# Performance work log

Hardware: AMD Instinct MI355X
Metric: run time of the kernel (lower is better)

## Reference

```python
import math
import jax, jax.numpy as jnp
import numpy as np

N = 2048
HID = 1024
ALPHA = 0.5
BETA = 0.1  # greedy term is zero when coords is None


def setup_inputs() -> dict:
    key = jax.random.key(0)
    k1, k2, k3, k4 = jax.random.split(key, 4)
    node_emb = jax.random.normal(k1, (N, HID), jnp.float32)
    demands = jax.random.uniform(k2, (N,), jnp.float32)  # each < 1 << capacity
    # query_net: Linear(hid+2 -> hid); key_net: Linear(hid -> hid)
    Wq = jax.random.normal(k3, (HID, HID + 2), jnp.float32) / math.sqrt(HID + 2)
    bq = jnp.zeros((HID,), jnp.float32)
    Wk = jax.random.normal(k4, (HID, HID), jnp.float32) / math.sqrt(HID)
    bk = jnp.zeros((HID,), jnp.float32)
    return {"node_emb": node_emb, "demands": demands, "Wq": Wq, "bq": bq,
            "Wk": Wk, "bk": bk, "capacity": 40, "depot_idx": 0}


def _decode(node_emb, demands, Wq, bq, Wk, bk, capacity, depot_idx):
    n, h = node_emb.shape
    cap = jnp.float32(capacity)
    inv_sqrt = 1.0 / math.sqrt(h)
    # key_net is a per-node linear map: precompute once (same math as per-step gather+linear)
    K = node_emb @ Wk.T + bk  # [N, H]
    idx = jnp.arange(n)
    # demands < 1, capacity = 40 => >= 39 customers per route => few depot returns;
    # T = N + N//8 safely bounds customer picks + route-closing depot emissions.
    T = n + n // 8
    visited0 = jnp.zeros((n,), bool).at[depot_idx].set(True)

    def step(carry, _):
        visited, load, last, done = carry
        feasible = (~visited) & (demands <= load)
        has_cand = jnp.any(feasible)
        # context = [emb(last), load/capacity, avgd]; avgd = 0 since coords is None
        ctx = jnp.concatenate([node_emb[last],
                               jnp.stack([load / cap, jnp.float32(0.0)])])
        q = Wq @ ctx + bq                      # [H]
        s = ALPHA * ((K @ q) * inv_sqrt)       # [N] scores over all nodes
        s_m = jnp.where(feasible, s, -jnp.inf)
        cand = jnp.argmax(s_m)
        take = has_cand & (~done)
        nxt = jnp.where(take, cand, depot_idx).astype(jnp.int32)
        step_score = jnp.where(take, s[cand], jnp.float32(0.0))
        visited = visited | ((idx == cand) & take)
        load = jnp.where(take, load - demands[cand], cap)  # route end resets load
        done = done | ((~take) & jnp.all(visited))
        return (visited, load, nxt, done), (nxt, step_score)

    carry0 = (visited0, cap, jnp.int32(depot_idx), jnp.bool_(False))
    _, (seq, scores) = jax.lax.scan(step, carry0, None, length=T)
    tour = jnp.concatenate([jnp.array([depot_idx], seq.dtype), seq])  # [T+1]
    return tour, scores


def reference(node_emb, demands, Wq, bq, Wk, bk, capacity, depot_idx):
    # tour: flat visitation order; routes are the segments between depot occurrences
    # (trailing depots are padding once all customers are served).
    # scores: selected decoder score at each step (0 at depot/padding steps).
    return _decode(node_emb, demands, Wq, bq, Wk, bk, capacity, depot_idx)
```

## Files before the change

kernel.cpp:

```cpp
#include <hip/hip_runtime.h>
#include <hip/hip_bf16.h>


#define NN 2048
#define HH 1024
#define TSTEPS (NN + NN / 8)
#define TILE 64
#define KT 16
#define KCAND 128

__global__ __launch_bounds__(256) void prep_wqh(const float* __restrict__ Wq,
                                                float* __restrict__ Wqh) {
  int id = blockIdx.x * 256 + threadIdx.x;
  int r = id >> 10, c = id & 1023;
  Wqh[id] = Wq[r * (HH + 2) + c];
}

__global__ __launch_bounds__(256) void gemm_nt(const float* __restrict__ A, int lda,
                                               const float* __restrict__ B, int ldb,
                                               float* __restrict__ C, int ldc,
                                               int K, const float* __restrict__ bias) {
  __shared__ float As[KT][TILE + 4];
  __shared__ float Bs[KT][TILE + 4];
  const int i0 = blockIdx.y * TILE;
  const int j0 = blockIdx.x * TILE;
  const int t = threadIdx.x;
  const int srow = t >> 2, sq = t & 3;
  const int tx = t & 15, ty = t >> 4;
  float acc[4][4] = {};
  for (int k0 = 0; k0 < K; k0 += KT) {
    float4 av = *(const float4*)&A[(size_t)(i0 + srow) * lda + k0 + sq * 4];
    float4 bv = *(const float4*)&B[(size_t)(j0 + srow) * ldb + k0 + sq * 4];
    __syncthreads();
    As[sq * 4 + 0][srow] = av.x; As[sq * 4 + 1][srow] = av.y;
    As[sq * 4 + 2][srow] = av.z; As[sq * 4 + 3][srow] = av.w;
    Bs[sq * 4 + 0][srow] = bv.x; Bs[sq * 4 + 1][srow] = bv.y;
    Bs[sq * 4 + 2][srow] = bv.z; Bs[sq * 4 + 3][srow] = bv.w;
    __syncthreads();
#pragma unroll
    for (int k = 0; k < KT; ++k) {
      float4 a4 = *(const float4*)&As[k][ty * 4];
      float4 b4 = *(const float4*)&Bs[k][tx * 4];
      float a[4] = {a4.x, a4.y, a4.z, a4.w};
      float b[4] = {b4.x, b4.y, b4.z, b4.w};
#pragma unroll
      for (int m = 0; m < 4; ++m)
#pragma unroll
        for (int n = 0; n < 4; ++n) acc[m][n] = fmaf(a[m], b[n], acc[m][n]);
    }
  }
  float bb[4] = {0.f, 0.f, 0.f, 0.f};
  if (bias) {
#pragma unroll
    for (int n = 0; n < 4; ++n) bb[n] = bias[j0 + tx * 4 + n];
  }
#pragma unroll
  for (int m = 0; m < 4; ++m) {
    float4 st = {acc[m][0] + bb[0], acc[m][1] + bb[1], acc[m][2] + bb[2], acc[m][3] + bb[3]};
    *(float4*)&C[(size_t)(i0 + ty * 4 + m) * ldc + j0 + tx * 4] = st;
  }
}

__global__ __launch_bounds__(64) void uv_k(const float* __restrict__ Kmat,
                                           const float* __restrict__ Wq,
                                           const float* __restrict__ bq,
                                           float* __restrict__ u, float* __restrict__ v) {
  int i = blockIdx.x;
  int lane = threadIdx.x;
  float su = 0.f, sv = 0.f;
#pragma unroll
  for (int m = 0; m < HH / 64; ++m) {
    int j = lane + 64 * m;
    float kv = Kmat[(size_t)i * HH + j];
    su = fmaf(kv, Wq[(size_t)j * (HH + 2) + HH], su);
    sv = fmaf(kv, bq[j], sv);
  }
#pragma unroll
  for (int off = 32; off; off >>= 1) {
    su += __shfl_down(su, off, 64);
    sv += __shfl_down(sv, off, 64);
  }
  if (lane == 0) { u[i] = su; v[i] = sv; }
}

__global__ __launch_bounds__(256) void umax_k(const float* __restrict__ u,
                                              float* __restrict__ umaxp) {
  __shared__ float sm[256];
  int t = threadIdx.x;
  float m = 0.f;
  for (int i = t; i < NN; i += 256) m = fmaxf(m, fabsf(u[i]));
  sm[t] = m;
  __syncthreads();
  for (int s = 128; s; s >>= 1) {
    if (t < s) sm[t] = fmaxf(sm[t], sm[t + s]);
    __syncthreads();
  }
  if (t == 0) *umaxp = sm[0];
}

__device__ __forceinline__ unsigned f2key(float f) {
  unsigned x = __float_as_uint(f);
  return x ^ ((x >> 31) ? 0xFFFFFFFFu : 0x80000000u);
}
__device__ __forceinline__ float key2f(unsigned k) {
  unsigned x = (k & 0x80000000u) ? (k ^ 0x80000000u) : ~k;
  return __uint_as_float(x);
}
__global__ __launch_bounds__(256) void prep_cand(const float* __restrict__ GT,
                                                 uint2* __restrict__ cand,
                                                 float* __restrict__ thr) {
  __shared__ float rowv[NN];
  __shared__ int hist[256];
  __shared__ int s_d, s_need, s_gt, s_eq;
  const int row = blockIdx.x, t = threadIdx.x;
  for (int i = t; i < NN; i += 256) rowv[i] = GT[(size_t)row * NN + i];
  __syncthreads();
  unsigned prefix = 0;
  int need = KCAND;
  for (int pass = 0; pass < 4; ++pass) {
    hist[t] = 0;
    __syncthreads();
    const int shift = 24 - 8 * pass;
    for (int i = t; i < NN; i += 256) {
      unsigned k = f2key(rowv[i]);
      if (pass == 0 || (k >> (shift + 8)) == (prefix >> (shift + 8)))
        atomicAdd(&hist[(k >> shift) & 0xFF], 1);
    }
    __syncthreads();
    if (t == 0) {
      int cum = 0, d = 255;
      for (; d > 0; --d) {
        if (cum + hist[d] >= need) break;
        cum += hist[d];
      }
      s_d = d;
      s_need = need - cum;
    }
    __syncthreads();
    prefix |= ((unsigned)s_d) << shift;
    need = s_need;
    __syncthreads();
  }
  const unsigned thrk = prefix;
  if (t == 0) { s_gt = 0; s_eq = 0; thr[row] = key2f(thrk); }
  __syncthreads();
  for (int i = t; i < NN; i += 256) {
    if (f2key(rowv[i]) > thrk) {
      int p = atomicAdd(&s_gt, 1);
      cand[(size_t)row * KCAND + p] = make_uint2(__float_as_uint(rowv[i]), (unsigned)i);
    }
  }
  __syncthreads();
  const int cgt = s_gt;
  for (int i = t; i < NN; i += 256) {
    if (f2key(rowv[i]) == thrk) {
      int p = atomicAdd(&s_eq, 1);
      if (p < KCAND - cgt)
        cand[(size_t)row * KCAND + cgt + p] = make_uint2(__float_as_uint(rowv[i]), (unsigned)i);
    }
  }
}

__global__ __launch_bounds__(256) void warm_k(const float* __restrict__ a, int n,
                                              const float* __restrict__ b, int m,
                                              float* __restrict__ sink) {
  float s = 0.f;
  const float4* a4 = (const float4*)a;
  for (int i = threadIdx.x; i < n / 4; i += 256) {
    float4 x = a4[i];
    s += x.x + x.y + x.z + x.w;
  }
  for (int i = threadIdx.x; i < m; i += 256) s += b[i];
  if (s == 1.2345e-30f) sink[blockIdx.x] = s;
}

#define DPP_MERGE2(CTRL)                                                      \
  {                                                                           \
    int ovb = __builtin_amdgcn_update_dpp(                                    \
        (int)0xFF800000, __float_as_int(bv), (CTRL), 0xf, 0xf, false);        \
    int oib = __builtin_amdgcn_update_dpp(                                    \
        0x7fffffff, bi, (CTRL), 0xf, 0xf, false);                             \
    float ov = __int_as_float(ovb);                                           \
    if (ov > bv || (ov == bv && oib < bi)) { bv = ov; bi = oib; }             \
  }

__global__ __launch_bounds__(64, 1) void decode(const float* __restrict__ GT,
                                                const uint2* __restrict__ cand,
                                                const float* __restrict__ thrp,
                                                const float* __restrict__ umaxp,
                                                const float* __restrict__ u,
                                                const float* __restrict__ demands,
                                                const int* __restrict__ capp,
                                                const int* __restrict__ depotp,
                                                float* __restrict__ out) {
  __shared__ __align__(16) float s_dem[NN];
  __shared__ __align__(16) float s_dd[NN];
  __shared__ __align__(16) float s_u[NN];
  __shared__ __align__(16) uint4 s_dcand[KCAND / 2];
  __shared__ __align__(16) float s_tour[TSTEPS + 1];
  __shared__ __align__(16) float s_lr[TSTEPS];

  const int lane = threadIdx.x;
  const int depot = *depotp;
  const float capf = (float)(*capp);
  const float umaxv = *umaxp;
  const float INF = __builtin_inff();
  const float NEGINF = -INF;
  const float C0 = 0.015625f;
  const float MARGIN = 0.5f;

  for (int i = lane; i < NN; i += 64) {
    float d = demands[i];
    s_dem[i] = d;
    s_dd[i] = d;
    s_u[i] = u[i];
  }
  const uint4* dc4 = (const uint4*)(cand + (size_t)depot * KCAND);
  for (int i = lane; i < KCAND / 2; i += 64) s_dcand[i] = dc4[i];
  const float thrd = thrp[depot];
  __syncthreads();
  if (lane == 0) {
    s_dd[depot] = INF;
    s_tour[0] = (float)depot;
  }

  float uu[32];
#pragma unroll
  for (int r = 0; r < 8; ++r) {
    float4 u4 = ((const float4*)u)[r * 64 + lane];
    uu[r * 4 + 0] = u4.x; uu[r * 4 + 1] = u4.y;
    uu[r * 4 + 2] = u4.z; uu[r * 4 + 3] = u4.w;
  }

  const float4* dd4 = (const float4*)s_dd;

  int done = 0, ntaken = 0, lasts = depot;
  float load = capf;
  float lr = load / capf;
  float thrcur = thrd;
  uint4 ca = dc4[lane];

  for (int step = 0; step < TSTEPS; ++step) {
    if (done) {
      const float df = (float)depot;
      for (int q = step + lane; q < TSTEPS; q += 64) {
        s_tour[1 + q] = df;
        s_lr[q] = -1.0f;
      }
      break;
    }
    float bv = NEGINF;
    int bi = 0x7fffffff;
    {
      float g0 = __uint_as_float(ca.x); int i0 = (int)ca.y;
      float g1 = __uint_as_float(ca.z); int i1 = (int)ca.w;
      float d0 = s_dd[i0], u0 = s_u[i0];
      float d1 = s_dd[i1], u1 = s_u[i1];
      float t0 = fmaf(u0, lr, g0);
      float t1 = fmaf(u1, lr, g1);
      if ((d0 <= load) && (t0 > bv || (t0 == bv && i0 < bi))) { bv = t0; bi = i0; }
      if ((d1 <= load) && (t1 > bv || (t1 == bv && i1 < bi))) { bv = t1; bi = i1; }
    }
    DPP_MERGE2(0x111); DPP_MERGE2(0x112); DPP_MERGE2(0x114);
    DPP_MERGE2(0x118); DPP_MERGE2(0x142); DPP_MERGE2(0x143);
    float rbv = __int_as_float(__builtin_amdgcn_readlane(__float_as_int(bv), 63));
    int rbi = __builtin_amdgcn_readlane(bi, 63);

    const float B = fmaf(lr, umaxv, thrcur) + MARGIN;
    int take, nxt;
    if (rbv > B) {
      take = 1; nxt = rbi;
    } else {
      const float4* rowp = (const float4*)(GT + (size_t)lasts * NN);
      float bv = NEGINF;
      int bi = NN;
#pragma unroll
      for (int r = 0; r < 8; ++r) {
        float4 g4 = rowp[r * 64 + lane];
        float4 d4 = dd4[r * 64 + lane];
        float gl[4] = {g4.x, g4.y, g4.z, g4.w};
        float dl[4] = {d4.x, d4.y, d4.z, d4.w};
        float cv = NEGINF;
        int cj = 0;
#pragma unroll
        for (int j = 0; j < 4; ++j) {
          float tt = fmaf(uu[r * 4 + j], lr, gl[j]);
          bool feas = (dl[j] <= load);
          if (feas && tt > cv) { cv = tt; cj = j; }
        }
        if (cv > bv) { bv = cv; bi = 4 * (r * 64 + lane) + cj; }
      }
      DPP_MERGE2(0x111); DPP_MERGE2(0x112); DPP_MERGE2(0x114);
      DPP_MERGE2(0x118); DPP_MERGE2(0x142); DPP_MERGE2(0x143);
      float fbv = __int_as_float(__builtin_amdgcn_readlane(__float_as_int(bv), 63));
      rbi = __builtin_amdgcn_readlane(bi, 63);
      take = (fbv > NEGINF);
      nxt = take ? rbi : depot;
    }

    if (nxt == depot) {
      ca = s_dcand[lane];
      thrcur = thrd;
    } else {
      const uint4* rc4 = (const uint4*)(cand + (size_t)nxt * KCAND);
      ca = rc4[lane];
      thrcur = thrp[nxt];
    }

    if (lane == 0) {
      s_tour[1 + step] = (float)nxt;
      s_lr[step] = take ? lr : -1.0f;
    }
    if (take) {
      load = load - s_dem[rbi];
      ntaken++;
      if (lane == 0) s_dd[rbi] = INF;
    } else {
      load = capf;
      if (ntaken == NN - 1) done = 1;
    }
    lasts = nxt;
    lr = load / capf;
  }

  for (int i = lane; i <= TSTEPS; i += 64) out[i] = s_tour[i];
  for (int s = lane; s < TSTEPS; s += 64) {
    float lrs = s_lr[s];
    float sc = 0.0f;
    if (lrs >= 0.0f) {
      int lastI = (int)s_tour[s];
      int biI = (int)s_tour[s + 1];
      float g = GT[(size_t)lastI * NN + biI];
      sc = fmaf(u[biI], lrs, g) * C0;
    }
    out[1 + TSTEPS + s] = sc;
  }
}

extern "C" void kernel_launch(void* const* d_in, const int* in_sizes, int n_in,
                              void* d_out, int out_size, void* d_ws, size_t ws_size,
                              hipStream_t stream) {
  const float* emb     = (const float*)d_in[0];
  const float* demands = (const float*)d_in[1];
  const float* Wq      = (const float*)d_in[2];
  const float* bq      = (const float*)d_in[3];
  const float* Wk      = (const float*)d_in[4];
  const float* bk      = (const float*)d_in[5];
  const int* cap       = (const int*)d_in[6];
  const int* depot     = (const int*)d_in[7];
  float* out           = (float*)d_out;

  char* ws = (char*)d_ws;
  float* Kmat = (float*)(ws);
  float* Z    = (float*)(ws + ((size_t)8 << 20));
  float* GT   = (float*)(ws + ((size_t)16 << 20));
  float* Wqh  = (float*)(ws + ((size_t)32 << 20));
  float* u    = (float*)(ws + ((size_t)36 << 20));
  float* v    = (float*)(ws + ((size_t)36 << 20) + 8192);
  float* thr  = (float*)(ws + ((size_t)36 << 20) + 16384);
  float* umax = (float*)(ws + ((size_t)36 << 20) + 24576);
  float* sink = (float*)(ws + ((size_t)36 << 20) + 32768);
  uint2* cnd  = (uint2*)Wqh;

  hipLaunchKernelGGL(prep_wqh, dim3(4096), dim3(256), 0, stream, Wq, Wqh);
  hipLaunchKernelGGL(gemm_nt, dim3(HH / TILE, NN / TILE), dim3(256), 0, stream,
                     emb, HH, Wk, HH, Kmat, HH, HH, bk);
  hipLaunchKernelGGL(gemm_nt, dim3(HH / TILE, NN / TILE), dim3(256), 0, stream,
                     emb, HH, Wqh, HH, Z, HH, HH, (const float*)nullptr);
  hipLaunchKernelGGL(uv_k, dim3(NN), dim3(64), 0, stream, Kmat, Wq, bq, u, v);
  hipLaunchKernelGGL(umax_k, dim3(1), dim3(256), 0, stream, u, umax);
  hipLaunchKernelGGL(gemm_nt, dim3(NN / TILE, NN / TILE), dim3(256), 0, stream,
                     Z, HH, Kmat, HH, GT, NN, HH, v);
  hipLaunchKernelGGL(prep_cand, dim3(NN), dim3(256), 0, stream, GT, cnd, thr);
  hipLaunchKernelGGL(warm_k, dim3(128), dim3(256), 0, stream,
                     (const float*)cnd, NN * KCAND * 2, thr, NN, sink);
  hipLaunchKernelGGL(decode, dim3(1), dim3(64), 0, stream, GT, cnd, thr, umax,
                     u, demands, cap, depot, out);
}
```

Measured before the change: 2.046 ms.

## Add bf16 top-5 per-row candidate tier in LDS before top-128 and full-row fallback

A new kernel builds each row's top-5 candidates, packed as bf16 score plus index, and decode keeps the whole table in LDS. Each step first tries a top-2 DPP merge over these five entries and accepts the winner only when it clears the runner-up and the 5th threshold by an error margin. Otherwise it falls back to the top-128 candidate list, now software-prefetched a step ahead, and then to the full row scan. This aims to cut the per-step global-memory latency on the serial decode path. The error margin and tie handling add correctness risk, and tour and score outputs now go through global buffers.

Measured after the change: 2.163 ms. +5.7%, slower.

```diff
diff --git a/kernel.cpp b/kernel.cpp
--- a/kernel.cpp
+++ b/kernel.cpp
@@ -7,7 +7,8 @@
 #define TSTEPS (NN + NN / 8)
 #define TILE 64
 #define KT 16
-#define KCAND 128
+#define KMID 128
+#define TSTR 6
 
 __global__ __launch_bounds__(256) void prep_wqh(const float* __restrict__ Wq,
                                                 float* __restrict__ Wqh) {
@@ -83,8 +84,16 @@
   if (lane == 0) { u[i] = su; v[i] = sv; }
 }
 
+__device__ __forceinline__ unsigned short f2bf_rn(float f) {
+  unsigned x = __float_as_uint(f);
+  unsigned r = ((x >> 16) & 1u) + 0x7fffu;
+  return (unsigned short)((x + r) >> 16);
+}
+
 __global__ __launch_bounds__(256) void umax_k(const float* __restrict__ u,
-                                              float* __restrict__ umaxp) {
+                                              float* __restrict__ umaxp,
+                                              unsigned* __restrict__ gmaxA,
+                                              unsigned* __restrict__ ub16) {
   __shared__ float sm[256];
   int t = threadIdx.x;
   float m = 0.f;
@@ -95,7 +104,9 @@
     if (t < s) sm[t] = fmaxf(sm[t], sm[t + s]);
     __syncthreads();
   }
-  if (t == 0) *umaxp = sm[0];
+  if (t == 0) { *umaxp = sm[0]; *gmaxA = 0u; }
+  for (int i = t; i < NN / 2; i += 256)
+    ub16[i] = (unsigned)f2bf_rn(u[2 * i]) | ((unsigned)f2bf_rn(u[2 * i + 1]) << 16);
 }
 
 __device__ __forceinline__ unsigned f2key(float f) {
@@ -116,7 +127,7 @@
   for (int i = t; i < NN; i += 256) rowv[i] = GT[(size_t)row * NN + i];
   __syncthreads();
   unsigned prefix = 0;
-  int need = KCAND;
+  int need = KMID;
   for (int pass = 0; pass < 4; ++pass) {
     hist[t] = 0;
     __syncthreads();
@@ -147,7 +158,7 @@
   for (int i = t; i < NN; i += 256) {
     if (f2key(rowv[i]) > thrk) {
       int p = atomicAdd(&s_gt, 1);
-      cand[(size_t)row * KCAND + p] = make_uint2(__float_as_uint(rowv[i]), (unsigned)i);
+      cand[(size_t)row * KMID + p] = make_uint2(__float_as_uint(rowv[i]), (unsigned)i);
     }
   }
   __syncthreads();
@@ -155,10 +166,46 @@
   for (int i = t; i < NN; i += 256) {
     if (f2key(rowv[i]) == thrk) {
       int p = atomicAdd(&s_eq, 1);
-      if (p < KCAND - cgt)
-        cand[(size_t)row * KCAND + cgt + p] = make_uint2(__float_as_uint(rowv[i]), (unsigned)i);
-    }
-  }
+      if (p < KMID - cgt)
+        cand[(size_t)row * KMID + cgt + p] = make_uint2(__float_as_uint(rowv[i]), (unsigned)i);
+    }
+  }
+}
+
+#define DPP_MERGE2(CTRL)                                                      \
+  {                                                                           \
+    int ovb = __builtin_amdgcn_update_dpp(                                    \
+        (int)0xFF800000, __float_as_int(bv), (CTRL), 0xf, 0xf, false);        \
+    int oib = __builtin_amdgcn_update_dpp(                                    \
+        0x7fffffff, bi, (CTRL), 0xf, 0xf, false);                             \
+    float ov = __int_as_float(ovb);                                           \
+    if (ov > bv || (ov == bv && oib < bi)) { bv = ov; bi = oib; }             \
+  }
+
+__global__ __launch_bounds__(64) void prep_top5(const uint2* __restrict__ cand,
+                                                unsigned* __restrict__ c5,
+                                                unsigned* __restrict__ gmaxA) {
+  const int row = blockIdx.x, lane = threadIdx.x;
+  uint2 e0 = cand[(size_t)row * KMID + lane];
+  uint2 e1 = cand[(size_t)row * KMID + 64 + lane];
+  float g0 = __uint_as_float(e0.x), g1 = __uint_as_float(e1.x);
+  float am = 0.f;
+  for (int k = 0; k < 5; ++k) {
+    float bv; int bi;
+    if (g0 >= g1) { bv = g0; bi = lane * 2; } else { bv = g1; bi = lane * 2 + 1; }
+    DPP_MERGE2(0x111); DPP_MERGE2(0x112); DPP_MERGE2(0x114);
+    DPP_MERGE2(0x118); DPP_MERGE2(0x142); DPP_MERGE2(0x143);
+    float wv = __int_as_float(__builtin_amdgcn_readlane(__float_as_int(bv), 63));
+    int wenc = __builtin_amdgcn_readlane(bi, 63);
+    if (lane == (wenc >> 1)) {
+      unsigned idx = (wenc & 1) ? e1.y : e0.y;
+      c5[row * TSTR + k] = ((unsigned)f2bf_rn(wv) << 16) | (idx & 0xffffu);
+      if (k == 4) c5[row * TSTR + 5] = __float_as_uint(wv);
+      if (wenc & 1) g1 = -__builtin_inff(); else g0 = -__builtin_inff();
+    }
+    am = fmaxf(am, fabsf(wv));
+  }
+  if (lane == 0) atomicMax(gmaxA, __float_as_uint(am));
 }
 
 __global__ __launch_bounds__(256) void warm_k(const float* __restrict__ a, int n,
@@ -174,55 +221,55 @@
   if (s == 1.2345e-30f) sink[blockIdx.x] = s;
 }
 
-#define DPP_MERGE2(CTRL)                                                      \
+#define TOP2_MERGE(CTRL)                                                      \
   {                                                                           \
-    int ovb = __builtin_amdgcn_update_dpp(                                    \
-        (int)0xFF800000, __float_as_int(bv), (CTRL), 0xf, 0xf, false);        \
-    int oib = __builtin_amdgcn_update_dpp(                                    \
-        0x7fffffff, bi, (CTRL), 0xf, 0xf, false);                             \
-    float ov = __int_as_float(ovb);                                           \
-    if (ov > bv || (ov == bv && oib < bi)) { bv = ov; bi = oib; }             \
+    int ov1b = __builtin_amdgcn_update_dpp(                                   \
+        (int)0xFF800000, __float_as_int(v1), (CTRL), 0xf, 0xf, false);        \
+    int oi1b = __builtin_amdgcn_update_dpp(                                   \
+        0x7fffffff, i1, (CTRL), 0xf, 0xf, false);                             \
+    int ov2b = __builtin_amdgcn_update_dpp(                                   \
+        (int)0xFF800000, __float_as_int(v2), (CTRL), 0xf, 0xf, false);        \
+    float ov1 = __int_as_float(ov1b), ov2 = __int_as_float(ov2b);             \
+    float vmax = fmaxf(v1, ov1), vmin = fminf(v1, ov1);                       \
+    v2 = fmaxf(vmin, fmaxf(v2, ov2));                                         \
+    i1 = (ov1 > v1) ? oi1b : ((ov1 < v1) ? i1 : min(i1, oi1b));               \
+    v1 = vmax;                                                                \
   }
 
 __global__ __launch_bounds__(64, 1) void decode(const float* __restrict__ GT,
                                                 const uint2* __restrict__ cand,
                                                 const float* __restrict__ thrp,
+                                                const unsigned* __restrict__ c5g,
+                                                const unsigned* __restrict__ ub16,
+                                                const unsigned* __restrict__ gmaxA,
                                                 const float* __restrict__ umaxp,
                                                 const float* __restrict__ u,
                                                 const float* __restrict__ demands,
                                                 const int* __restrict__ capp,
                                                 const int* __restrict__ depotp,
+                                                int* __restrict__ tourW,
+                                                float* __restrict__ lrW,
                                                 float* __restrict__ out) {
-  __shared__ __align__(16) float s_dem[NN];
+  __shared__ __align__(16) unsigned s_c5[NN * TSTR];
   __shared__ __align__(16) float s_dd[NN];
-  __shared__ __align__(16) float s_u[NN];
-  __shared__ __align__(16) uint4 s_dcand[KCAND / 2];
-  __shared__ __align__(16) float s_tour[TSTEPS + 1];
-  __shared__ __align__(16) float s_lr[TSTEPS];
+  __shared__ __align__(16) unsigned short s_ub[NN];
 
   const int lane = threadIdx.x;
   const int depot = *depotp;
   const float capf = (float)(*capp);
   const float umaxv = *umaxp;
+  const float gmaxv = __uint_as_float(*gmaxA);
   const float INF = __builtin_inff();
   const float NEGINF = -INF;
   const float C0 = 0.015625f;
-  const float MARGIN = 0.5f;
-
-  for (int i = lane; i < NN; i += 64) {
-    float d = demands[i];
-    s_dem[i] = d;
-    s_dd[i] = d;
-    s_u[i] = u[i];
-  }
-  const uint4* dc4 = (const uint4*)(cand + (size_t)depot * KCAND);
-  for (int i = lane; i < KCAND / 2; i += 64) s_dcand[i] = dc4[i];
-  const float thrd = thrp[depot];
+  const float EPST = (gmaxv + umaxv) * 0.0021f + 0.02f;
+
+  for (int i = lane; i < NN * TSTR / 4; i += 64)
+    ((uint4*)s_c5)[i] = ((const uint4*)c5g)[i];
+  for (int i = lane; i < NN; i += 64) s_dd[i] = demands[i];
+  for (int i = lane; i < NN / 2; i += 64) ((unsigned*)s_ub)[i] = ub16[i];
   __syncthreads();
-  if (lane == 0) {
-    s_dd[depot] = INF;
-    s_tour[0] = (float)depot;
-  }
+  if (lane == 0) s_dd[depot] = INF;
 
   float uu[32];
 #pragma unroll
@@ -231,107 +278,125 @@
     uu[r * 4 + 0] = u4.x; uu[r * 4 + 1] = u4.y;
     uu[r * 4 + 2] = u4.z; uu[r * 4 + 3] = u4.w;
   }
-
   const float4* dd4 = (const float4*)s_dd;
 
   int done = 0, ntaken = 0, lasts = depot;
   float load = capf;
   float lr = load / capf;
-  float thrcur = thrd;
-  uint4 ca = dc4[lane];
+
+  uint4 pf0 = *(const uint4*)(cand + (size_t)depot * KMID + lane * 2);
+  uint4 pf1 = pf0;
+  float thr0 = thrp[depot], thr1 = thr0;
 
   for (int step = 0; step < TSTEPS; ++step) {
     if (done) {
-      const float df = (float)depot;
       for (int q = step + lane; q < TSTEPS; q += 64) {
-        s_tour[1 + q] = df;
-        s_lr[q] = -1.0f;
+        tourW[q] = depot;
+        lrW[q] = -1.0f;
       }
       break;
     }
-    float bv = NEGINF;
-    int bi = 0x7fffffff;
-    {
-      float g0 = __uint_as_float(ca.x); int i0 = (int)ca.y;
-      float g1 = __uint_as_float(ca.z); int i1 = (int)ca.w;
-      float d0 = s_dd[i0], u0 = s_u[i0];
-      float d1 = s_dd[i1], u1 = s_u[i1];
-      float t0 = fmaf(u0, lr, g0);
-      float t1 = fmaf(u1, lr, g1);
-      if ((d0 <= load) && (t0 > bv || (t0 == bv && i0 < bi))) { bv = t0; bi = i0; }
-      if ((d1 <= load) && (t1 > bv || (t1 == bv && i1 < bi))) { bv = t1; bi = i1; }
-    }
-    DPP_MERGE2(0x111); DPP_MERGE2(0x112); DPP_MERGE2(0x114);
-    DPP_MERGE2(0x118); DPP_MERGE2(0x142); DPP_MERGE2(0x143);
-    float rbv = __int_as_float(__builtin_amdgcn_readlane(__float_as_int(bv), 63));
-    int rbi = __builtin_amdgcn_readlane(bi, 63);
-
-    const float B = fmaf(lr, umaxv, thrcur) + MARGIN;
+    unsigned w = 0;
+    if (lane < 6) w = s_c5[lasts * TSTR + lane];
+    float v1 = NEGINF, v2 = NEGINF;
+    int i1 = 0x7fffffff;
+    if (lane < 5) {
+      int idx = (int)(w & 0xffffu);
+      float gh = __uint_as_float(w & 0xffff0000u);
+      float uh = __uint_as_float(((unsigned)s_ub[idx]) << 16);
+      float d = s_dd[idx];
+      float t = fmaf(uh, lr, gh);
+      if (d <= load) { v1 = t; i1 = idx; }
+    }
+    TOP2_MERGE(0x111); TOP2_MERGE(0x112); TOP2_MERGE(0x114);
+    const float s1 = __int_as_float(__builtin_amdgcn_readlane(__float_as_int(v1), 7));
+    const float s2 = __int_as_float(__builtin_amdgcn_readlane(__float_as_int(v2), 7));
+    const int si = __builtin_amdgcn_readlane(i1, 7);
+    const float thr5v = __uint_as_float(__builtin_amdgcn_readlane((int)w, 5));
+    const float slack = fmaf(lr, umaxv, 0.5f) + EPST;
+
     int take, nxt;
-    if (rbv > B) {
-      take = 1; nxt = rbi;
+    if (s1 - EPST > s2 + EPST && s1 - EPST > thr5v + slack) {
+      take = 1; nxt = si;
     } else {
-      const float4* rowp = (const float4*)(GT + (size_t)lasts * NN);
+      const uint4 c4 = (step & 1) ? pf1 : pf0;
+      const float thrm = (step & 1) ? thr1 : thr0;
       float bv = NEGINF;
-      int bi = NN;
-#pragma unroll
-      for (int r = 0; r < 8; ++r) {
-        float4 g4 = rowp[r * 64 + lane];
-        float4 d4 = dd4[r * 64 + lane];
-        float gl[4] = {g4.x, g4.y, g4.z, g4.w};
-        float dl[4] = {d4.x, d4.y, d4.z, d4.w};
-        float cv = NEGINF;
-        int cj = 0;
-#pragma unroll
-        for (int j = 0; j < 4; ++j) {
-          float tt = fmaf(uu[r * 4 + j], lr, gl[j]);
-          bool feas = (dl[j] <= load);
-          if (feas && tt > cv) { cv = tt; cj = j; }
-        }
-        if (cv > bv) { bv = cv; bi = 4 * (r * 64 + lane) + cj; }
+      int bi = 0x7fffffff;
+      {
+        float g0 = __uint_as_float(c4.x); int j0 = (int)c4.y;
+        float g1 = __uint_as_float(c4.z); int j1 = (int)c4.w;
+        float d0 = s_dd[j0], d1 = s_dd[j1];
+        float ue0 = u[j0], ue1 = u[j1];
+        float t0 = fmaf(ue0, lr, g0);
+        float t1 = fmaf(ue1, lr, g1);
+        if ((d0 <= load) && (t0 > bv || (t0 == bv && j0 < bi))) { bv = t0; bi = j0; }
+        if ((d1 <= load) && (t1 > bv || (t1 == bv && j1 < bi))) { bv = t1; bi = j1; }
       }
       DPP_MERGE2(0x111); DPP_MERGE2(0x112); DPP_MERGE2(0x114);
       DPP_MERGE2(0x118); DPP_MERGE2(0x142); DPP_MERGE2(0x143);
-      float fbv = __int_as_float(__builtin_amdgcn_readlane(__float_as_int(bv), 63));
-      rbi = __builtin_amdgcn_readlane(bi, 63);
-      take = (fbv > NEGINF);
-      nxt = take ? rbi : depot;
-    }
-
-    if (nxt == depot) {
-      ca = s_dcand[lane];
-      thrcur = thrd;
-    } else {
-      const uint4* rc4 = (const uint4*)(cand + (size_t)nxt * KCAND);
-      ca = rc4[lane];
-      thrcur = thrp[nxt];
-    }
-
-    if (lane == 0) {
-      s_tour[1 + step] = (float)nxt;
-      s_lr[step] = take ? lr : -1.0f;
-    }
+      float rbv = __int_as_float(__builtin_amdgcn_readlane(__float_as_int(bv), 63));
+      int rbi = __builtin_amdgcn_readlane(bi, 63);
+      if (rbv > fmaf(lr, umaxv, thrm) + 0.5f) {
+        take = 1; nxt = rbi;
+      } else {
+        const float4* rowp = (const float4*)(GT + (size_t)lasts * NN);
+        float bv = NEGINF;
+        int bi = NN;
+#pragma unroll
+        for (int r = 0; r < 8; ++r) {
+          float4 g4 = rowp[r * 64 + lane];
+          float4 d4 = dd4[r * 64 + lane];
+          float gl[4] = {g4.x, g4.y, g4.z, g4.w};
+          float dl[4] = {d4.x, d4.y, d4.z, d4.w};
+          float cv = NEGINF;
+          int cj = 0;
+#pragma unroll
+          for (int j = 0; j < 4; ++j) {
+            float tt = fmaf(uu[r * 4 + j], lr, gl[j]);
+            bool feas = (dl[j] <= load);
+            if (feas && tt > cv) { cv = tt; cj = j; }
+          }
+          if (cv > bv) { bv = cv; bi = 4 * (r * 64 + lane) + cj; }
+        }
+        DPP_MERGE2(0x111); DPP_MERGE2(0x112); DPP_MERGE2(0x114);
+        DPP_MERGE2(0x118); DPP_MERGE2(0x142); DPP_MERGE2(0x143);
+        float fbv = __int_as_float(__builtin_amdgcn_readlane(__float_as_int(bv), 63));
+        int fbi = __builtin_amdgcn_readlane(bi, 63);
+        take = (fbv > NEGINF);
+        nxt = take ? fbi : depot;
+      }
+    }
+
+    if (lane == 0) { tourW[step] = nxt; lrW[step] = take ? lr : -1.0f; }
     if (take) {
-      load = load - s_dem[rbi];
+      float dsel = s_dd[nxt];
+      load = load - dsel;
       ntaken++;
-      if (lane == 0) s_dd[rbi] = INF;
+      if (lane == 0) s_dd[nxt] = INF;
     } else {
       load = capf;
       if (ntaken == NN - 1) done = 1;
     }
     lasts = nxt;
     lr = load / capf;
-  }
-
-  for (int i = lane; i <= TSTEPS; i += 64) out[i] = s_tour[i];
+
+    uint4 npf = *(const uint4*)(cand + (size_t)lasts * KMID + lane * 2);
+    float nthr = thrp[lasts];
+    if (step & 1) { pf0 = npf; thr0 = nthr; } else { pf1 = npf; thr1 = nthr; }
+  }
+
+  __threadfence();
+  if (lane == 0) out[0] = (float)depot;
   for (int s = lane; s < TSTEPS; s += 64) {
-    float lrs = s_lr[s];
+    int nx = tourW[s];
+    out[1 + s] = (float)nx;
+    float lrs = lrW[s];
     float sc = 0.0f;
     if (lrs >= 0.0f) {
-      int lastI = (int)s_tour[s];
-      int biI = (int)s_tour[s + 1];
-      float g = GT[(size_t)lastI * NN + biI];
-      sc = fmaf(u[biI], lrs, g) * C0;
+      int lastI = (s == 0) ? depot : tourW[s - 1];
+      float g = GT[(size_t)lastI * NN + nx];
+      sc = fmaf(u[nx], lrs, g) * C0;
     }
     out[1 + TSTEPS + s] = sc;
   }
@@ -355,12 +420,18 @@
   float* Z    = (float*)(ws + ((size_t)8 << 20));
   float* GT   = (float*)(ws + ((size_t)16 << 20));
   float* Wqh  = (float*)(ws + ((size_t)32 << 20));
-  float* u    = (float*)(ws + ((size_t)36 << 20));
-  float* v    = (float*)(ws + ((size_t)36 << 20) + 8192);
-  float* thr  = (float*)(ws + ((size_t)36 << 20) + 16384);
-  float* umax = (float*)(ws + ((size_t)36 << 20) + 24576);
-  float* sink = (float*)(ws + ((size_t)36 << 20) + 32768);
-  uint2* cnd  = (uint2*)Wqh;
+  char* ex    = ws + ((size_t)36 << 20);
+  float* u      = (float*)(ex);
+  float* v      = (float*)(ex + 8192);
+  float* thr    = (float*)(ex + 16384);
+  float* umax   = (float*)(ex + 24576);
+  unsigned* gmaxA = (unsigned*)(ex + 24704);
+  float* sink   = (float*)(ex + 24832);
+  unsigned* ub16 = (unsigned*)(ex + 32768);
+  unsigned* c5g  = (unsigned*)(ex + 40960);
+  int* tourW    = (int*)(ex + 40960 + 49152);
+  float* lrW    = (float*)(ex + 40960 + 49152 + 9216);
+  uint2* cnd    = (uint2*)Wqh;
 
   hipLaunchKernelGGL(prep_wqh, dim3(4096), dim3(256), 0, stream, Wq, Wqh);
   hipLaunchKernelGGL(gemm_nt, dim3(HH / TILE, NN / TILE), dim3(256), 0, stream,
@@ -368,12 +439,13 @@
   hipLaunchKernelGGL(gemm_nt, dim3(HH / TILE, NN / TILE), dim3(256), 0, stream,
                      emb, HH, Wqh, HH, Z, HH, HH, (const float*)nullptr);
   hipLaunchKernelGGL(uv_k, dim3(NN), dim3(64), 0, stream, Kmat, Wq, bq, u, v);
-  hipLaunchKernelGGL(umax_k, dim3(1), dim3(256), 0, stream, u, umax);
+  hipLaunchKernelGGL(umax_k, dim3(1), dim3(256), 0, stream, u, umax, gmaxA, ub16);
   hipLaunchKernelGGL(gemm_nt, dim3(NN / TILE, NN / TILE), dim3(256), 0, stream,
                      Z, HH, Kmat, HH, GT, NN, HH, v);
   hipLaunchKernelGGL(prep_cand, dim3(NN), dim3(256), 0, stream, GT, cnd, thr);
+  hipLaunchKernelGGL(prep_top5, dim3(NN), dim3(64), 0, stream, cnd, c5g, gmaxA);
   hipLaunchKernelGGL(warm_k, dim3(128), dim3(256), 0, stream,
-                     (const float*)cnd, NN * KCAND * 2, thr, NN, sink);
-  hipLaunchKernelGGL(decode, dim3(1), dim3(64), 0, stream, GT, cnd, thr, umax,
-                     u, demands, cap, depot, out);
-}
+                     (const float*)cnd, NN * KMID * 2, thr, NN, sink);
+  hipLaunchKernelGGL(decode, dim3(1), dim3(64), 0, stream, GT, cnd, thr, c5g,
+                     ub16, gmaxA, umax, u, demands, cap, depot, tourW, lrW, out);
+}
```

## Pack u and demand into candidate records and prefetch via async LDS loads

Applied to the files above, without the earlier changes.

Candidate entries grow to 16 bytes holding score, index, u and demand, so the decode loop no longer does dependent LDS lookups of u and demand per candidate. The next row's candidates are pulled with global_load_lds into a double buffer in shared memory. Visited state moves to a bitmask, thresholds are read from shared memory, and the tour and lr arrays move from LDS to global scratch. This doubles candidate memory and the warm-up footprint, and the serial decode still waits on vmcnt(0) every step.

After: 2.469 ms. +20.7%, slower.

```diff
diff --git a/kernel.cpp b/kernel.cpp
--- a/kernel.cpp
+++ b/kernel.cpp
@@ -7,7 +7,7 @@
 #define TSTEPS (NN + NN / 8)
 #define TILE 64
 #define KT 16
-#define KCAND 128
+#define KMID 128
 
 __global__ __launch_bounds__(256) void prep_wqh(const float* __restrict__ Wq,
                                                 float* __restrict__ Wqh) {
@@ -107,7 +107,9 @@
   return __uint_as_float(x);
 }
 __global__ __launch_bounds__(256) void prep_cand(const float* __restrict__ GT,
-                                                 uint2* __restrict__ cand,
+                                                 const float* __restrict__ u,
+                                                 const float* __restrict__ dem,
+                                                 uint4* __restrict__ cand,
                                                  float* __restrict__ thr) {
   __shared__ float rowv[NN];
   __shared__ int hist[256];
@@ -116,7 +118,7 @@
   for (int i = t; i < NN; i += 256) rowv[i] = GT[(size_t)row * NN + i];
   __syncthreads();
   unsigned prefix = 0;
-  int need = KCAND;
+  int need = KMID;
   for (int pass = 0; pass < 4; ++pass) {
     hist[t] = 0;
     __syncthreads();
@@ -147,7 +149,9 @@
   for (int i = t; i < NN; i += 256) {
     if (f2key(rowv[i]) > thrk) {
       int p = atomicAdd(&s_gt, 1);
-      cand[(size_t)row * KCAND + p] = make_uint2(__float_as_uint(rowv[i]), (unsigned)i);
+      cand[(size_t)row * KMID + p] =
+          make_uint4(__float_as_uint(rowv[i]), (unsigned)i,
+                     __float_as_uint(u[i]), __float_as_uint(dem[i]));
     }
   }
   __syncthreads();
@@ -155,8 +159,10 @@
   for (int i = t; i < NN; i += 256) {
     if (f2key(rowv[i]) == thrk) {
       int p = atomicAdd(&s_eq, 1);
-      if (p < KCAND - cgt)
-        cand[(size_t)row * KCAND + cgt + p] = make_uint2(__float_as_uint(rowv[i]), (unsigned)i);
+      if (p < KMID - cgt)
+        cand[(size_t)row * KMID + cgt + p] =
+            make_uint4(__float_as_uint(rowv[i]), (unsigned)i,
+                       __float_as_uint(u[i]), __float_as_uint(dem[i]));
     }
   }
 }
@@ -184,21 +190,27 @@
     if (ov > bv || (ov == bv && oib < bi)) { bv = ov; bi = oib; }             \
   }
 
+__device__ __forceinline__ void gload_lds16(const uint4* g, uint4* l) {
+  __builtin_amdgcn_global_load_lds(
+      (const __attribute__((address_space(1))) void*)g,
+      (__attribute__((address_space(3))) void*)l, 16, 0, 0);
+}
+
 __global__ __launch_bounds__(64, 1) void decode(const float* __restrict__ GT,
-                                                const uint2* __restrict__ cand,
+                                                const uint4* __restrict__ cand,
                                                 const float* __restrict__ thrp,
                                                 const float* __restrict__ umaxp,
                                                 const float* __restrict__ u,
                                                 const float* __restrict__ demands,
                                                 const int* __restrict__ capp,
                                                 const int* __restrict__ depotp,
+                                                int* __restrict__ tourW,
+                                                float* __restrict__ lrW,
                                                 float* __restrict__ out) {
-  __shared__ __align__(16) float s_dem[NN];
   __shared__ __align__(16) float s_dd[NN];
-  __shared__ __align__(16) float s_u[NN];
-  __shared__ __align__(16) uint4 s_dcand[KCAND / 2];
-  __shared__ __align__(16) float s_tour[TSTEPS + 1];
-  __shared__ __align__(16) float s_lr[TSTEPS];
+  __shared__ __align__(16) float s_thr[NN];
+  __shared__ __align__(16) unsigned s_vis[NN / 32];
+  __shared__ __align__(16) uint4 s_pf[2][KMID];
 
   const int lane = threadIdx.x;
   const int depot = *depotp;
@@ -207,21 +219,18 @@
   const float INF = __builtin_inff();
   const float NEGINF = -INF;
   const float C0 = 0.015625f;
-  const float MARGIN = 0.5f;
 
   for (int i = lane; i < NN; i += 64) {
-    float d = demands[i];
-    s_dem[i] = d;
-    s_dd[i] = d;
-    s_u[i] = u[i];
-  }
-  const uint4* dc4 = (const uint4*)(cand + (size_t)depot * KCAND);
-  for (int i = lane; i < KCAND / 2; i += 64) s_dcand[i] = dc4[i];
-  const float thrd = thrp[depot];
+    s_dd[i] = demands[i];
+    s_thr[i] = thrp[i];
+  }
+  if (lane == 0) {
+    for (int i = 0; i < NN / 32; ++i) s_vis[i] = 0xFFFFFFFFu;
+  }
   __syncthreads();
   if (lane == 0) {
     s_dd[depot] = INF;
-    s_tour[0] = (float)depot;
+    s_vis[depot >> 5] &= ~(1u << (depot & 31));
   }
 
   float uu[32];
@@ -231,44 +240,49 @@
     uu[r * 4 + 0] = u4.x; uu[r * 4 + 1] = u4.y;
     uu[r * 4 + 2] = u4.z; uu[r * 4 + 3] = u4.w;
   }
-
   const float4* dd4 = (const float4*)s_dd;
 
   int done = 0, ntaken = 0, lasts = depot;
   float load = capf;
   float lr = load / capf;
-  float thrcur = thrd;
-  uint4 ca = dc4[lane];
+
+  gload_lds16(cand + (size_t)depot * KMID + lane, &s_pf[0][0]);
+  gload_lds16(cand + (size_t)depot * KMID + 64 + lane, &s_pf[0][64]);
 
   for (int step = 0; step < TSTEPS; ++step) {
     if (done) {
-      const float df = (float)depot;
       for (int q = step + lane; q < TSTEPS; q += 64) {
-        s_tour[1 + q] = df;
-        s_lr[q] = -1.0f;
+        tourW[q] = depot;
+        lrW[q] = -1.0f;
       }
       break;
     }
+    const int par = step & 1;
+    asm volatile("s_waitcnt vmcnt(0)" ::: "memory");
+    uint4 e0 = s_pf[par][lane];
+    uint4 e1 = s_pf[par][64 + lane];
+
     float bv = NEGINF;
     int bi = 0x7fffffff;
     {
-      float g0 = __uint_as_float(ca.x); int i0 = (int)ca.y;
-      float g1 = __uint_as_float(ca.z); int i1 = (int)ca.w;
-      float d0 = s_dd[i0], u0 = s_u[i0];
-      float d1 = s_dd[i1], u1 = s_u[i1];
+      float g0 = __uint_as_float(e0.x); int j0 = (int)e0.y;
+      float u0 = __uint_as_float(e0.z); float d0 = __uint_as_float(e0.w);
+      float g1 = __uint_as_float(e1.x); int j1 = (int)e1.y;
+      float u1 = __uint_as_float(e1.z); float d1 = __uint_as_float(e1.w);
+      bool f0 = (d0 <= load) && ((s_vis[j0 >> 5] >> (j0 & 31)) & 1u);
+      bool f1 = (d1 <= load) && ((s_vis[j1 >> 5] >> (j1 & 31)) & 1u);
       float t0 = fmaf(u0, lr, g0);
       float t1 = fmaf(u1, lr, g1);
-      if ((d0 <= load) && (t0 > bv || (t0 == bv && i0 < bi))) { bv = t0; bi = i0; }
-      if ((d1 <= load) && (t1 > bv || (t1 == bv && i1 < bi))) { bv = t1; bi = i1; }
+      if (f0 && (t0 > bv || (t0 == bv && j0 < bi))) { bv = t0; bi = j0; }
+      if (f1 && (t1 > bv || (t1 == bv && j1 < bi))) { bv = t1; bi = j1; }
     }
     DPP_MERGE2(0x111); DPP_MERGE2(0x112); DPP_MERGE2(0x114);
     DPP_MERGE2(0x118); DPP_MERGE2(0x142); DPP_MERGE2(0x143);
     float rbv = __int_as_float(__builtin_amdgcn_readlane(__float_as_int(bv), 63));
     int rbi = __builtin_amdgcn_readlane(bi, 63);
 
-    const float B = fmaf(lr, umaxv, thrcur) + MARGIN;
     int take, nxt;
-    if (rbv > B) {
+    if (rbv > fmaf(lr, umaxv, s_thr[lasts]) + 0.5f) {
       take = 1; nxt = rbi;
     } else {
       const float4* rowp = (const float4*)(GT + (size_t)lasts * NN);
@@ -293,28 +307,26 @@
       DPP_MERGE2(0x111); DPP_MERGE2(0x112); DPP_MERGE2(0x114);
       DPP_MERGE2(0x118); DPP_MERGE2(0x142); DPP_MERGE2(0x143);
       float fbv = __int_as_float(__builtin_amdgcn_readlane(__float_as_int(bv), 63));
-      rbi = __builtin_amdgcn_readlane(bi, 63);
+      int fbi = __builtin_amdgcn_readlane(bi, 63);
       take = (fbv > NEGINF);
-      nxt = take ? rbi : depot;
-    }
-
-    if (nxt == depot) {
-      ca = s_dcand[lane];
-      thrcur = thrd;
-    } else {
-      const uint4* rc4 = (const uint4*)(cand + (size_t)nxt * KCAND);
-      ca = rc4[lane];
-      thrcur = thrp[nxt];
-    }
-
-    if (lane == 0) {
-      s_tour[1 + step] = (float)nxt;
-      s_lr[step] = take ? lr : -1.0f;
-    }
+      nxt = take ? fbi : depot;
+    }
+
+    {
+      const uint4* gsrc = cand + (size_t)nxt * KMID + lane;
+      gload_lds16(gsrc, &s_pf[par ^ 1][0]);
+      gload_lds16(gsrc + 64, &s_pf[par ^ 1][64]);
+    }
+
+    if (lane == 0) { tourW[step] = nxt; lrW[step] = take ? lr : -1.0f; }
     if (take) {
-      load = load - s_dem[rbi];
+      float dsel = s_dd[nxt];
+      load = load - dsel;
       ntaken++;
-      if (lane == 0) s_dd[rbi] = INF;
+      if (lane == 0) {
+        s_dd[nxt] = INF;
+        s_vis[nxt >> 5] &= ~(1u << (nxt & 31));
+      }
     } else {
       load = capf;
       if (ntaken == NN - 1) done = 1;
@@ -323,15 +335,17 @@
     lr = load / capf;
   }
 
-  for (int i = lane; i <= TSTEPS; i += 64) out[i] = s_tour[i];
+  __threadfence();
+  if (lane == 0) out[0] = (float)depot;
   for (int s = lane; s < TSTEPS; s += 64) {
-    float lrs = s_lr[s];
+    int nx = tourW[s];
+    out[1 + s] = (float)nx;
+    float lrs = lrW[s];
     float sc = 0.0f;
     if (lrs >= 0.0f) {
-      int lastI = (int)s_tour[s];
-      int biI = (int)s_tour[s + 1];
-      float g = GT[(size_t)lastI * NN + biI];
-      sc = fmaf(u[biI], lrs, g) * C0;
+      int lastI = (s == 0) ? depot : tourW[s - 1];
+      float g = GT[(size_t)lastI * NN + nx];
+      sc = fmaf(u[nx], lrs, g) * C0;
     }
     out[1 + TSTEPS + s] = sc;
   }
@@ -355,12 +369,15 @@
   float* Z    = (float*)(ws + ((size_t)8 << 20));
   float* GT   = (float*)(ws + ((size_t)16 << 20));
   float* Wqh  = (float*)(ws + ((size_t)32 << 20));
-  float* u    = (float*)(ws + ((size_t)36 << 20));
-  float* v    = (float*)(ws + ((size_t)36 << 20) + 8192);
-  float* thr  = (float*)(ws + ((size_t)36 << 20) + 16384);
-  float* umax = (float*)(ws + ((size_t)36 << 20) + 24576);
-  float* sink = (float*)(ws + ((size_t)36 << 20) + 32768);
-  uint2* cnd  = (uint2*)Wqh;
+  char* ex    = ws + ((size_t)36 << 20);
+  float* u      = (float*)(ex);
+  float* v      = (float*)(ex + 8192);
+  float* thr    = (float*)(ex + 16384);
+  float* umax   = (float*)(ex + 24576);
+  float* sink   = (float*)(ex + 24832);
+  int* tourW    = (int*)(ex + 40960);
+  float* lrW    = (float*)(ex + 40960 + 9216);
+  uint4* cnd    = (uint4*)Wqh;
 
   hipLaunchKernelGGL(prep_wqh, dim3(4096), dim3(256), 0, stream, Wq, Wqh);
   hipLaunchKernelGGL(gemm_nt, dim3(HH / TILE, NN / TILE), dim3(256), 0, stream,
@@ -371,9 +388,10 @@
   hipLaunchKernelGGL(umax_k, dim3(1), dim3(256), 0, stream, u, umax);
   hipLaunchKernelGGL(gemm_nt, dim3(NN / TILE, NN / TILE), dim3(256), 0, stream,
                      Z, HH, Kmat, HH, GT, NN, HH, v);
-  hipLaunchKernelGGL(prep_cand, dim3(NN), dim3(256), 0, stream, GT, cnd, thr);
+  hipLaunchKernelGGL(prep_cand, dim3(NN), dim3(256), 0, stream, GT, u, demands,
+                     cnd, thr);
   hipLaunchKernelGGL(warm_k, dim3(128), dim3(256), 0, stream,
-                     (const float*)cnd, NN * KCAND * 2, thr, NN, sink);
+                     (const float*)cnd, NN * KMID * 4, thr, NN, sink);
   hipLaunchKernelGGL(decode, dim3(1), dim3(64), 0, stream, GT, cnd, thr, umax,
-                     u, demands, cap, depot, out);
-}
+                     u, demands, cap, depot, tourW, lrW, out);
+}
```
